# Kernel optimization log

Hardware: AMD Instinct MI355X
Metric: run time of the kernel (lower is better)

## Reference

```python
import jax, jax.numpy as jnp
import numpy as np

NUM_HEADS = 16
DIM = 1280
HEAD_DIM = DIM // NUM_HEADS  # 80
N_TOKENS = 4096


def _rotate_half(x):
    x1, x2 = jnp.split(x, 2, axis=-1)
    return jnp.concatenate([-x2, x1], axis=-1)


def _apply_rotary_vision(t, freqs):
    # t: (N, H, D), freqs: (N, D//2)
    cos = jnp.tile(jnp.cos(freqs), (1, 2))[:, None, :]  # (N, 1, D)
    sin = jnp.tile(jnp.sin(freqs), (1, 2))[:, None, :]
    return t * cos + _rotate_half(t) * sin


def setup_inputs() -> dict:
    key = jax.random.key(0)
    ks = jax.random.split(key, 6)
    hidden_states = jax.random.normal(ks[0], (N_TOKENS, DIM), dtype=jnp.float32)
    # 4 packed variable-length image sequences
    cu_seqlens = jnp.array([0, 600, 1600, 2800, N_TOKENS], dtype=jnp.int32)
    rotary_pos_emb = jax.random.normal(ks[1], (N_TOKENS, HEAD_DIM // 2), dtype=jnp.float32)
    w_qkv = jax.random.normal(ks[2], (DIM, 3 * DIM), dtype=jnp.float32) * 0.02
    b_qkv = jax.random.normal(ks[3], (3 * DIM,), dtype=jnp.float32) * 0.02
    w_proj = jax.random.normal(ks[4], (DIM, DIM), dtype=jnp.float32) * 0.02
    b_proj = jax.random.normal(ks[5], (DIM,), dtype=jnp.float32) * 0.02
    return {"hidden_states": hidden_states, "cu_seqlens": cu_seqlens,
            "rotary_pos_emb": rotary_pos_emb, "w_qkv": w_qkv, "b_qkv": b_qkv,
            "w_proj": w_proj, "b_proj": b_proj}


def reference(hidden_states, cu_seqlens, rotary_pos_emb, w_qkv, b_qkv, w_proj, b_proj):
    N = hidden_states.shape[0]
    H, D = NUM_HEADS, HEAD_DIM
    qkv = hidden_states @ w_qkv + b_qkv                  # (N, 3*dim)
    qkv = qkv.reshape(N, 3, H, D)
    q, k, v = qkv[:, 0], qkv[:, 1], qkv[:, 2]            # (N, H, D)
    q = _apply_rotary_vision(q, rotary_pos_emb)
    k = _apply_rotary_vision(k, rotary_pos_emb)
    # segment id per token from cu_seqlens boundaries
    pos = jnp.arange(N, dtype=jnp.int32)
    seg = jnp.searchsorted(cu_seqlens, pos, side='right') - 1  # (N,)
    same_seg = seg[:, None] == seg[None, :]              # (N, N) bool
    scale = 1.0 / jnp.sqrt(jnp.asarray(D, dtype=q.dtype))
    scores = jnp.einsum('nhd,mhd->hnm', q, k) * scale    # (H, N, N)
    scores = jnp.where(same_seg[None, :, :], scores, jnp.finfo(scores.dtype).min)
    probs = jax.nn.softmax(scores, axis=-1)
    out = jnp.einsum('hnm,mhd->nhd', probs, v)           # (N, H, D)
    out = out.reshape(N, H * D)
    return out @ w_proj + b_proj
```

## Files before the change

kernel.cpp:

```cpp
#include <hip/hip_runtime.h>
#include <math.h>


#define N_TOK 4096
#define DIMM  1280
#define NHEAD 16
#define HD    80
#define QKVN  3840
#define KP    3840

typedef short bf16x8 __attribute__((ext_vector_type(8)));
typedef float f32x4  __attribute__((ext_vector_type(4)));

__device__ __forceinline__ unsigned short f2bf(float x) {
    unsigned int u = __float_as_uint(x);
    u += 0x7fff + ((u >> 16) & 1);
    return (unsigned short)(u >> 16);
}
__device__ __forceinline__ float bf2f(unsigned short h) {
    return __uint_as_float(((unsigned int)h) << 16);
}
__device__ __forceinline__ void gload_lds16(const void* g, void* l) {
    __builtin_amdgcn_global_load_lds(
        (const __attribute__((address_space(1))) unsigned int*)g,
        (__attribute__((address_space(3))) unsigned int*)l, 16, 0, 0);
}

#define MFMA16(a, b, c) __builtin_amdgcn_mfma_f32_16x16x32_bf16((a), (b), (c), 0, 0, 0)

__global__ void pack_A_kernel(const float* __restrict__ X, unsigned short* __restrict__ Ap)
{
    const int idx = blockIdx.x * blockDim.x + threadIdx.x;
    if (idx >= N_TOK * DIMM / 4) return;
    const int e = idx * 4;
    const int m = e / DIMM, k = e - (e / DIMM) * DIMM;
    const float4 v = *reinterpret_cast<const float4*>(&X[(size_t)m * DIMM + k]);
    ushort4 hi, lo;
    hi.x = f2bf(v.x); lo.x = f2bf(v.x - bf2f(hi.x));
    hi.y = f2bf(v.y); lo.y = f2bf(v.y - bf2f(hi.y));
    hi.z = f2bf(v.z); lo.z = f2bf(v.z - bf2f(hi.z));
    hi.w = f2bf(v.w); lo.w = f2bf(v.w - bf2f(hi.w));
    const size_t base = (size_t)m * KP + k;
    *reinterpret_cast<ushort4*>(&Ap[base])            = hi;
    *reinterpret_cast<ushort4*>(&Ap[base + DIMM])     = lo;
    *reinterpret_cast<ushort4*>(&Ap[base + 2 * DIMM]) = hi;
}

__global__ __launch_bounds__(256)
void pack_Bt_kernel(const float* __restrict__ W, unsigned short* __restrict__ Bt, int Ncols)
{
    __shared__ float Ts[32][33];
    const int k0 = blockIdx.x * 32, n0 = blockIdx.y * 32;
    const int t = threadIdx.x;
    const int r = t >> 3, c4 = (t & 7) * 4;
    const float4 v = *reinterpret_cast<const float4*>(&W[(size_t)(k0 + r) * Ncols + n0 + c4]);
    Ts[r][c4] = v.x; Ts[r][c4 + 1] = v.y; Ts[r][c4 + 2] = v.z; Ts[r][c4 + 3] = v.w;
    __syncthreads();
    float w0 = Ts[c4][r], w1 = Ts[c4 + 1][r], w2 = Ts[c4 + 2][r], w3 = Ts[c4 + 3][r];
    ushort4 hi, lo;
    hi.x = f2bf(w0); lo.x = f2bf(w0 - bf2f(hi.x));
    hi.y = f2bf(w1); lo.y = f2bf(w1 - bf2f(hi.y));
    hi.z = f2bf(w2); lo.z = f2bf(w2 - bf2f(hi.z));
    hi.w = f2bf(w3); lo.w = f2bf(w3 - bf2f(hi.w));
    const size_t base = (size_t)(n0 + r) * KP + k0 + c4;
    *reinterpret_cast<ushort4*>(&Bt[base])            = hi;
    *reinterpret_cast<ushort4*>(&Bt[base + DIMM])     = hi;
    *reinterpret_cast<ushort4*>(&Bt[base + 2 * DIMM]) = lo;
}

template<int EPI>
__global__ __launch_bounds__(256)
void gemm_mfma(const unsigned short* __restrict__ A, const unsigned short* __restrict__ Bt,
               const float* __restrict__ bias, float* __restrict__ out, int Ncols)
{
    __shared__ unsigned short As[128 * 32];
    __shared__ unsigned short Bs[128 * 32];

    const int tid  = threadIdx.x;
    const int w    = tid >> 6, lane = tid & 63;

    const int lin = blockIdx.x;
    const int x   = lin & 7;
    const int l   = lin >> 3;
    int m0, n0;
    if (EPI == 1) {
        m0 = ((x >> 1) * 8 + (l & 7)) * 128;
        n0 = ((x & 1) * 15 + (l >> 3)) * 128;
    } else {
        m0 = (x * 4 + (l & 3)) * 128;
        n0 = (l >> 2) * 128;
    }

    const int wm   = w >> 1, wn = w & 1;
    const int lm   = lane & 15, kb = lane >> 4;

    const char* Ag = (const char*)(A  + (size_t)(m0 + w * 32 + (lane >> 2)) * KP) + (lane & 3) * 16;
    const char* Bg = (const char*)(Bt + (size_t)(n0 + w * 32 + (lane >> 2)) * KP) + (lane & 3) * 16;
    char* AsB = (char*)As + w * 2048;
    char* BsB = (char*)Bs + w * 2048;
    const size_t rowskip = (size_t)16 * KP * 2;

    f32x4 acc[4][4] = {};

    for (int k0 = 0; k0 < KP; k0 += 32) {
        const size_t kb2 = (size_t)k0 * 2;
        gload_lds16(Ag + kb2,           AsB);
        gload_lds16(Ag + kb2 + rowskip, AsB + 1024);
        gload_lds16(Bg + kb2,           BsB);
        gload_lds16(Bg + kb2 + rowskip, BsB + 1024);
        __syncthreads();

        bf16x8 a[4], b[4];
        #pragma unroll
        for (int mf = 0; mf < 4; ++mf)
            a[mf] = *reinterpret_cast<const bf16x8*>(&As[(wm * 64 + mf * 16 + lm) * 32 + kb * 8]);
        #pragma unroll
        for (int nf = 0; nf < 4; ++nf)
            b[nf] = *reinterpret_cast<const bf16x8*>(&Bs[(wn * 64 + nf * 16 + lm) * 32 + kb * 8]);
        #pragma unroll
        for (int mf = 0; mf < 4; ++mf)
            #pragma unroll
            for (int nf = 0; nf < 4; ++nf)
                acc[mf][nf] = MFMA16(a[mf], b[nf], acc[mf][nf]);
        __syncthreads();
    }

    #pragma unroll
    for (int nf = 0; nf < 4; ++nf) {
        const int col = n0 + wn * 64 + nf * 16 + lm;
        const float bb = bias[col];
        #pragma unroll
        for (int mf = 0; mf < 4; ++mf) {
            #pragma unroll
            for (int r = 0; r < 4; ++r) {
                const int row = m0 + wm * 64 + mf * 16 + kb * 4 + r;
                const float c = acc[mf][nf][r] + bb;
                if (EPI == 0) {
                    out[(size_t)row * Ncols + col] = c;
                } else {
                    const int part = col / DIMM;
                    const int rem  = col - part * DIMM;
                    const int hh   = rem / HD;
                    const int d    = rem - hh * HD;
                    out[(((size_t)(part * NHEAD + hh)) * N_TOK + row) * HD + d] = c;
                }
            }
        }
    }
}

__global__ void rope_kernel(const float* __restrict__ freqs, float* __restrict__ q,
                            const float* __restrict__ k, unsigned short* __restrict__ Kpk)
{
    const int idx = blockIdx.x * blockDim.x + threadIdx.x;
    if (idx >= N_TOK * NHEAD * 40) return;
    const int dp = idx % 40;
    const int t  = idx / 40;
    const int h  = t & 15;
    const int n  = t >> 4;

    const float f = freqs[n * 40 + dp];
    const float c = cosf(f);
    const float s = sinf(f);

    const size_t base = ((size_t)h * N_TOK + n) * HD;
    const float q1 = q[base + dp], q2 = q[base + dp + 40];
    q[base + dp]      = q1 * c - q2 * s;
    q[base + dp + 40] = q2 * c + q1 * s;

    const float scale = 0.11180339887498949f;
    const float k1 = k[base + dp], k2 = k[base + dp + 40];
    const float kr1 = (k1 * c - k2 * s) * scale;
    const float kr2 = (k2 * c + k1 * s) * scale;

    const int tile = n >> 5, r = n & 31;
    const size_t hi = ((size_t)(h * 128 + tile) * 2 + 0) * 3328 + r * 104;
    const size_t lo = ((size_t)(h * 128 + tile) * 2 + 1) * 3328 + r * 104;
    const unsigned short h1 = f2bf(kr1);
    Kpk[hi + dp]      = h1;
    Kpk[lo + dp]      = f2bf(kr1 - bf2f(h1));
    const unsigned short h2 = f2bf(kr2);
    Kpk[hi + dp + 40] = h2;
    Kpk[lo + dp + 40] = f2bf(kr2 - bf2f(h2));
    if (dp < 12) {
        Kpk[hi + 80 + dp] = 0; Kpk[hi + 92 + dp] = 0;
        Kpk[lo + 80 + dp] = 0; Kpk[lo + 92 + dp] = 0;
    }
}

__global__ __launch_bounds__(256)
void vpack_kernel(const float* __restrict__ v, unsigned short* __restrict__ Vt)
{
    __shared__ float T[32][81];
    const int t = blockIdx.x, h = blockIdx.y;
    const int kt = t * 32;
    for (int e = threadIdx.x; e < 32 * 80; e += 256) {
        const int key = e / 80, d = e - (e / 80) * 80;
        T[key][d] = v[((size_t)h * N_TOK + kt + key) * HD + d];
    }
    __syncthreads();
    unsigned short* base = Vt + ((size_t)h * 128 + t) * 6400;
    for (int e = threadIdx.x; e < 3200; e += 256) {
        const int d = e / 40, col = e - (e / 40) * 40;
        float x = 0.f;
        if (col < 32) {
            const int key = (((col & 7) < 4) ? 0 : 16) + 4 * (col >> 3) + (col & 3);
            x = T[key][d];
        }
        const unsigned short hi = f2bf(x);
        base[e]        = hi;
        base[3200 + e] = f2bf(x - bf2f(hi));
    }
}

__global__ __launch_bounds__(512, 4)
void attn_mfma(const float* __restrict__ qbuf, const unsigned short* __restrict__ Kpk,
               const unsigned short* __restrict__ Vt, const int* __restrict__ cu,
               unsigned short* __restrict__ Ap)
{
    __shared__ __align__(16) unsigned short KS[2][6656];
    __shared__ __align__(16) unsigned short VS[2][6400];

    const int tid  = threadIdx.x;
    const int w    = tid >> 6, lane = tid & 63;
    const int lm   = lane & 15, g = lane >> 4;

    const int lin = blockIdx.x;
    const int h   = (lin & 7) * 2 + ((lin >> 3) & 1);
    const int q0  = (lin >> 4) * 128;

    const int c1 = cu[1], c2 = cu[2], c3 = cu[3];
    #define SEGOF(n) ((int)((n) >= c1) + (int)((n) >= c2) + (int)((n) >= c3))
    const int seg_first = SEGOF(q0);
    const int seg_last  = SEGOF(q0 + 127);
    const int cuv[5] = {0, c1, c2, c3, N_TOK};
    const int kmin = cuv[seg_first], kmax = cuv[seg_last + 1];
    const int kt0 = kmin & ~31;
    const int t0  = kt0 >> 5;
    const int ntiles = (kmax - kt0 + 31) >> 5;

    const size_t hb = (size_t)h * N_TOK;

    bf16x8 qh[3], ql[3];
    const int qrow = q0 + w * 16 + lm;
    {
        const float* qp = qbuf + (hb + qrow) * HD;
        #pragma unroll
        for (int ks = 0; ks < 3; ++ks) {
            #pragma unroll
            for (int j = 0; j < 8; ++j) {
                const int d = ks * 32 + g * 8 + j;
                const float x = (d < HD) ? qp[d] : 0.f;
                const unsigned short hi = f2bf(x);
                qh[ks][j] = (short)hi;
                ql[ks][j] = (short)f2bf(x - bf2f(hi));
            }
        }
    }
    const int sq  = SEGOF(qrow);
    const int klo = cuv[sq], khi = cuv[sq + 1];

    float mrow = -1e30f, lrow = 0.f;
    f32x4 accO[5] = {};

    auto issue = [&](int buf, int tg) {
        const char* sK = (const char*)(Kpk + ((size_t)(h * 128 + tg) * 2) * 3328);
        const char* sV = (const char*)(Vt  +  (size_t)(h * 128 + tg) * 6400);
        char* dK = (char*)&KS[buf][0];
        char* dV = (char*)&VS[buf][0];
        for (int j = w; j < 26; j += 8) {
            if (j < 13) {
                gload_lds16(sK + j * 1024 + (size_t)lane * 16, dK + j * 1024);
            } else if (j < 25) {
                gload_lds16(sV + (j - 13) * 1024 + (size_t)lane * 16, dV + (j - 13) * 1024);
            } else if (lane < 32) {
                gload_lds16(sV + 12288 + (size_t)lane * 16, dV + 12288);
            }
        }
    };

    issue(0, t0);
    if (ntiles > 1) issue(1, t0 + 1);

    for (int ti = 0; ti < ntiles; ++ti) {
        const int buf = ti & 1;
        const int kt  = kt0 + ti * 32;

        if (ti + 1 < ntiles) {
            if (w < 2) asm volatile("s_waitcnt vmcnt(4)" ::: "memory");
            else       asm volatile("s_waitcnt vmcnt(3)" ::: "memory");
        } else {
            asm volatile("s_waitcnt vmcnt(0)" ::: "memory");
        }
        __builtin_amdgcn_s_barrier();
        asm volatile("" ::: "memory");

        const unsigned short* Kb = &KS[buf][0];
        const unsigned short* Vb = &VS[buf][0];

        f32x4 s0 = {0.f, 0.f, 0.f, 0.f}, s1 = {0.f, 0.f, 0.f, 0.f};
        #pragma unroll
        for (int ks = 0; ks < 3; ++ks) {
            const bf16x8 k0h = *reinterpret_cast<const bf16x8*>(&Kb[lm * 104 + ks * 32 + g * 8]);
            const bf16x8 k0l = *reinterpret_cast<const bf16x8*>(&Kb[3328 + lm * 104 + ks * 32 + g * 8]);
            const bf16x8 k1h = *reinterpret_cast<const bf16x8*>(&Kb[(16 + lm) * 104 + ks * 32 + g * 8]);
            const bf16x8 k1l = *reinterpret_cast<const bf16x8*>(&Kb[3328 + (16 + lm) * 104 + ks * 32 + g * 8]);
            s0 = MFMA16(k0h, qh[ks], s0);
            s0 = MFMA16(k0h, ql[ks], s0);
            s0 = MFMA16(k0l, qh[ks], s0);
            s1 = MFMA16(k1h, qh[ks], s1);
            s1 = MFMA16(k1h, ql[ks], s1);
            s1 = MFMA16(k1l, qh[ks], s1);
        }

        bool v0m[4], v1m[4];
        #pragma unroll
        for (int r = 0; r < 4; ++r) {
            const int j0 = kt + g * 4 + r;
            const int j1 = j0 + 16;
            v0m[r] = (j0 >= klo) && (j0 < khi);
            v1m[r] = (j1 >= klo) && (j1 < khi);
        }

        float tm = -1e30f;
        #pragma unroll
        for (int r = 0; r < 4; ++r)
            tm = fmaxf(tm, fmaxf(v0m[r] ? s0[r] : -1e30f, v1m[r] ? s1[r] : -1e30f));
        tm = fmaxf(tm, __shfl_xor(tm, 16));
        tm = fmaxf(tm, __shfl_xor(tm, 32));

        const bool defer = __all(tm <= mrow + 8.0f);
        if (!defer) {
            const float mn = fmaxf(mrow, tm);
            const float sc = __expf(mrow - mn);
            mrow = mn;
            lrow *= sc;
            float scq[4];
            #pragma unroll
            for (int r = 0; r < 4; ++r) scq[r] = __shfl(sc, ((lane >> 4) << 2) + r);
            #pragma unroll
            for (int f = 0; f < 5; ++f) {
                accO[f][0] *= scq[0]; accO[f][1] *= scq[1];
                accO[f][2] *= scq[2]; accO[f][3] *= scq[3];
            }
        }

        float p0[4], p1[4], rs = 0.f;
        #pragma unroll
        for (int r = 0; r < 4; ++r) {
            p0[r] = v0m[r] ? __expf(s0[r] - mrow) : 0.f;
            p1[r] = v1m[r] ? __expf(s1[r] - mrow) : 0.f;
            rs += p0[r] + p1[r];
        }
        rs += __shfl_xor(rs, 16);
        rs += __shfl_xor(rs, 32);
        lrow += rs;

        bf16x8 pa;
        pa[0] = (short)f2bf(p0[0]); pa[1] = (short)f2bf(p0[1]);
        pa[2] = (short)f2bf(p0[2]); pa[3] = (short)f2bf(p0[3]);
        pa[4] = (short)f2bf(p1[0]); pa[5] = (short)f2bf(p1[1]);
        pa[6] = (short)f2bf(p1[2]); pa[7] = (short)f2bf(p1[3]);

        #pragma unroll
        for (int f = 0; f < 5; ++f) {
            const bf16x8 vh = *reinterpret_cast<const bf16x8*>(&Vb[(f * 16 + lm) * 40 + g * 8]);
            const bf16x8 vl = *reinterpret_cast<const bf16x8*>(&Vb[3200 + (f * 16 + lm) * 40 + g * 8]);
            accO[f] = MFMA16(pa, vh, accO[f]);
            accO[f] = MFMA16(pa, vl, accO[f]);
        }

        asm volatile("s_waitcnt lgkmcnt(0)" ::: "memory");
        __builtin_amdgcn_s_barrier();
        asm volatile("" ::: "memory");
        if (ti + 2 < ntiles) issue(buf, t0 + ti + 2);
    }

    const float linv = 1.f / lrow;
    float invq[4];
    #pragma unroll
    for (int r = 0; r < 4; ++r) invq[r] = __shfl(linv, ((lane >> 4) << 2) + r);

    #pragma unroll
    for (int r = 0; r < 4; ++r) {
        const int n = q0 + w * 16 + g * 4 + r;
        const size_t rb = (size_t)n * KP + h * HD;
        #pragma unroll
        for (int f = 0; f < 5; ++f) {
            const float v = accO[f][r] * invq[r];
            const unsigned short hi = f2bf(v);
            const unsigned short lo = f2bf(v - bf2f(hi));
            Ap[rb + f * 16 + lm]            = hi;
            Ap[rb + DIMM + f * 16 + lm]     = lo;
            Ap[rb + 2 * DIMM + f * 16 + lm] = hi;
        }
    }
    #undef SEGOF
}

extern "C" void kernel_launch(void* const* d_in, const int* in_sizes, int n_in,
                              void* d_out, int out_size, void* d_ws, size_t ws_size,
                              hipStream_t stream)
{
    const float* hidden = (const float*)d_in[0];
    const int*   cu     = (const int*)  d_in[1];
    const float* rope   = (const float*)d_in[2];
    const float* w_qkv  = (const float*)d_in[3];
    const float* b_qkv  = (const float*)d_in[4];
    const float* w_proj = (const float*)d_in[5];
    const float* b_proj = (const float*)d_in[6];
    float*       out    = (float*)d_out;

    const size_t perbuf = (size_t)NHEAD * N_TOK * HD;
    float* qbuf = (float*)d_ws;
    float* kbuf = qbuf + perbuf;
    float* vbuf = kbuf + perbuf;
    unsigned short* Apack = (unsigned short*)(vbuf + perbuf);
    unsigned short* BtQ   = Apack + (size_t)N_TOK * KP;
    unsigned short* BtP   = BtQ + (size_t)QKVN * KP;
    unsigned short* Vt    = BtP + (size_t)DIMM * KP;
    unsigned short* Kpk   = BtQ;

    pack_A_kernel<<<(N_TOK * DIMM / 4 + 255) / 256, 256, 0, stream>>>(hidden, Apack);
    pack_Bt_kernel<<<dim3(DIMM / 32, QKVN / 32), 256, 0, stream>>>(w_qkv, BtQ, QKVN);
    pack_Bt_kernel<<<dim3(DIMM / 32, DIMM / 32), 256, 0, stream>>>(w_proj, BtP, DIMM);

    gemm_mfma<1><<<960, 256, 0, stream>>>(Apack, BtQ, b_qkv, qbuf, QKVN);

    rope_kernel<<<(N_TOK * NHEAD * 40 + 255) / 256, 256, 0, stream>>>(rope, qbuf, kbuf, Kpk);
    vpack_kernel<<<dim3(128, NHEAD), 256, 0, stream>>>(vbuf, Vt);

    attn_mfma<<<512, 512, 0, stream>>>(qbuf, Kpk, Vt, cu, Apack);

    gemm_mfma<0><<<320, 256, 0, stream>>>(Apack, BtP, b_proj, out, DIMM);
}
```

Measured before the change: 548.9 us.

## Halve attention query tile to 64 rows, use exp2 softmax and packed bf16 convert

The attention kernel now uses 64-query tiles with 4 waves per block and 1024 blocks, changing the load issue loop and the vmcnt waits to match. The aim is finer segment bounds and better balance across CUs, at the cost of reloading K/V tiles more often. The K scale now folds in log2(e) so the softmax can use hardware exp2, and the deferral threshold is widened to match. P is converted with the packed v_cvt_pk_bf16_f32 instruction, and the output projection GEMM's tile mapping is reordered.

```diff
diff --git a/kernel.cpp b/kernel.cpp
--- a/kernel.cpp
+++ b/kernel.cpp
@@ -25,8 +25,14 @@
         (const __attribute__((address_space(1))) unsigned int*)g,
         (__attribute__((address_space(3))) unsigned int*)l, 16, 0, 0);
 }
+__device__ __forceinline__ unsigned int cvtpk_bf16(float a, float b) {
+    unsigned int r;
+    asm("v_cvt_pk_bf16_f32 %0, %1, %2" : "=v"(r) : "v"(a), "v"(b));
+    return r;
+}
 
 #define MFMA16(a, b, c) __builtin_amdgcn_mfma_f32_16x16x32_bf16((a), (b), (c), 0, 0, 0)
+#define EXP2(x) __builtin_amdgcn_exp2f(x)
 
 __global__ void pack_A_kernel(const float* __restrict__ X, unsigned short* __restrict__ Ap)
 {
@@ -87,8 +93,9 @@
         m0 = ((x >> 1) * 8 + (l & 7)) * 128;
         n0 = ((x & 1) * 15 + (l >> 3)) * 128;
     } else {
-        m0 = (x * 4 + (l & 3)) * 128;
-        n0 = (l >> 2) * 128;
+        const int wg = x * 40 + l;
+        m0 = (wg & 31) * 128;
+        n0 = (wg >> 5) * 128;
     }
 
     const int wm   = w >> 1, wn = w & 1;
@@ -168,7 +175,7 @@
     q[base + dp]      = q1 * c - q2 * s;
     q[base + dp + 40] = q2 * c + q1 * s;
 
-    const float scale = 0.11180339887498949f;
+    const float scale = 0.16129820579f;
     const float k1 = k[base + dp], k2 = k[base + dp + 40];
     const float kr1 = (k1 * c - k2 * s) * scale;
     const float kr2 = (k2 * c + k1 * s) * scale;
@@ -213,7 +220,7 @@
     }
 }
 
-__global__ __launch_bounds__(512, 4)
+__global__ __launch_bounds__(256)
 void attn_mfma(const float* __restrict__ qbuf, const unsigned short* __restrict__ Kpk,
                const unsigned short* __restrict__ Vt, const int* __restrict__ cu,
                unsigned short* __restrict__ Ap)
@@ -226,13 +233,13 @@
     const int lm   = lane & 15, g = lane >> 4;
 
     const int lin = blockIdx.x;
-    const int h   = (lin & 7) * 2 + ((lin >> 3) & 1);
-    const int q0  = (lin >> 4) * 128;
+    const int h   = (lin & 7) * 2 + (lin >> 9);
+    const int q0  = ((lin >> 3) & 63) * 64;
 
     const int c1 = cu[1], c2 = cu[2], c3 = cu[3];
     #define SEGOF(n) ((int)((n) >= c1) + (int)((n) >= c2) + (int)((n) >= c3))
     const int seg_first = SEGOF(q0);
-    const int seg_last  = SEGOF(q0 + 127);
+    const int seg_last  = SEGOF(q0 + 63);
     const int cuv[5] = {0, c1, c2, c3, N_TOK};
     const int kmin = cuv[seg_first], kmax = cuv[seg_last + 1];
     const int kt0 = kmin & ~31;
@@ -268,7 +275,7 @@
         const char* sV = (const char*)(Vt  +  (size_t)(h * 128 + tg) * 6400);
         char* dK = (char*)&KS[buf][0];
         char* dV = (char*)&VS[buf][0];
-        for (int j = w; j < 26; j += 8) {
+        for (int j = w; j < 26; j += 4) {
             if (j < 13) {
                 gload_lds16(sK + j * 1024 + (size_t)lane * 16, dK + j * 1024);
             } else if (j < 25) {
@@ -287,8 +294,8 @@
         const int kt  = kt0 + ti * 32;
 
         if (ti + 1 < ntiles) {
-            if (w < 2) asm volatile("s_waitcnt vmcnt(4)" ::: "memory");
-            else       asm volatile("s_waitcnt vmcnt(3)" ::: "memory");
+            if (w < 2) asm volatile("s_waitcnt vmcnt(7)" ::: "memory");
+            else       asm volatile("s_waitcnt vmcnt(6)" ::: "memory");
         } else {
             asm volatile("s_waitcnt vmcnt(0)" ::: "memory");
         }
@@ -329,10 +336,10 @@
         tm = fmaxf(tm, __shfl_xor(tm, 16));
         tm = fmaxf(tm, __shfl_xor(tm, 32));
 
-        const bool defer = __all(tm <= mrow + 8.0f);
+        const bool defer = __all(tm <= mrow + 11.5f);
         if (!defer) {
             const float mn = fmaxf(mrow, tm);
-            const float sc = __expf(mrow - mn);
+            const float sc = EXP2(mrow - mn);
             mrow = mn;
             lrow *= sc;
             float scq[4];
@@ -348,19 +355,20 @@
         float p0[4], p1[4], rs = 0.f;
         #pragma unroll
         for (int r = 0; r < 4; ++r) {
-            p0[r] = v0m[r] ? __expf(s0[r] - mrow) : 0.f;
-            p1[r] = v1m[r] ? __expf(s1[r] - mrow) : 0.f;
+            p0[r] = v0m[r] ? EXP2(s0[r] - mrow) : 0.f;
+            p1[r] = v1m[r] ? EXP2(s1[r] - mrow) : 0.f;
             rs += p0[r] + p1[r];
         }
         rs += __shfl_xor(rs, 16);
         rs += __shfl_xor(rs, 32);
         lrow += rs;
 
-        bf16x8 pa;
-        pa[0] = (short)f2bf(p0[0]); pa[1] = (short)f2bf(p0[1]);
-        pa[2] = (short)f2bf(p0[2]); pa[3] = (short)f2bf(p0[3]);
-        pa[4] = (short)f2bf(p1[0]); pa[5] = (short)f2bf(p1[1]);
-        pa[6] = (short)f2bf(p1[2]); pa[7] = (short)f2bf(p1[3]);
+        union { unsigned int u[4]; bf16x8 v; } pau;
+        pau.u[0] = cvtpk_bf16(p0[0], p0[1]);
+        pau.u[1] = cvtpk_bf16(p0[2], p0[3]);
+        pau.u[2] = cvtpk_bf16(p1[0], p1[1]);
+        pau.u[3] = cvtpk_bf16(p1[2], p1[3]);
+        const bf16x8 pa = pau.v;
 
         #pragma unroll
         for (int f = 0; f < 5; ++f) {
@@ -430,7 +438,7 @@
     rope_kernel<<<(N_TOK * NHEAD * 40 + 255) / 256, 256, 0, stream>>>(rope, qbuf, kbuf, Kpk);
     vpack_kernel<<<dim3(128, NHEAD), 256, 0, stream>>>(vbuf, Vt);
 
-    attn_mfma<<<512, 512, 0, stream>>>(qbuf, Kpk, Vt, cu, Apack);
+    attn_mfma<<<1024, 256, 0, stream>>>(qbuf, Kpk, Vt, cu, Apack);
 
     gemm_mfma<0><<<320, 256, 0, stream>>>(Apack, BtP, b_proj, out, DIMM);
 }
```

Measured after the change: 597.4 us. 1.09x slower.
